# Performance work log

Hardware: AMD Instinct MI355X
Metric: run time of the kernel (lower is better)

Reference implementation:

```python
import jax, jax.numpy as jnp
import numpy as np

B, S, H = 32, 2048, 512

def setup_inputs() -> dict:
    key = jax.random.key(0)
    k1, k2, k3, k4 = jax.random.split(key, 4)
    Y = jax.random.normal(k1, (B, S, H), dtype=jnp.float32)
    mask_Y = jnp.ones((B, S), dtype=jnp.float32)
    W = jax.random.normal(k2, (H, H), dtype=jnp.float32)
    b = jax.random.normal(k3, (H,), dtype=jnp.float32)
    w = jax.random.normal(k4, (H,), dtype=jnp.float32)
    return {"Y": Y, "mask_Y": mask_Y, "W": W, "b": b, "w": w}

def reference(Y, mask_Y, W, b, w):
    # u: [B,S,H] = tanh(Y @ W + b)
    u = jnp.tanh(jnp.einsum('bsh,hd->bsd', Y, W) + b)
    # scores: [B,S] = u . w, masked with large negative additive bias
    scores = jnp.einsum('bsh,h->bs', u, w) - 1000.0 * (1.0 - mask_Y)
    alpha = jax.nn.softmax(scores, axis=1)  # [B,S]
    # c_star: [B,H] = attention-weighted sum of Y
    c_star = jnp.einsum('bs,bsh->bh', alpha, Y)
    return c_star
```

## Files before the change

kernel.cpp:

```cpp
#include <hip/hip_runtime.h>
#include <hip/hip_bf16.h>


#define Bsz 32
#define Ssz 2048
#define Hsz 512
#define Msz (Bsz * Ssz)

using half8   = __attribute__((ext_vector_type(8))) _Float16;
using floatx4 = __attribute__((ext_vector_type(4))) float;

__device__ __forceinline__ void llds16(void* l, const void* g) {
  __builtin_amdgcn_global_load_lds((const __attribute__((address_space(1))) void*)g,
                                   (__attribute__((address_space(3))) void*)l, 16, 0, 0);
}

__device__ __forceinline__ float fast_tanh(float x) {
  const float e = __expf(2.f * x);
  return 1.f - 2.f / (e + 1.f);
}

__global__ __launch_bounds__(256) void wsplit_k(const float* __restrict__ W,
                                                _Float16* __restrict__ Wt) {
  __shared__ float tile[32][33];
  const int bx = blockIdx.x & 15, by = blockIdx.x >> 4;
  const int tx = threadIdx.x & 31, ty = threadIdx.x >> 5;
#pragma unroll
  for (int i = 0; i < 4; ++i)
    tile[ty + 8 * i][tx] = W[(size_t)(by * 32 + ty + 8 * i) * Hsz + bx * 32 + tx];
  __syncthreads();
#pragma unroll
  for (int i = 0; i < 4; ++i) {
    const int n = bx * 32 + ty + 8 * i;
    const int k = by * 32 + tx;
    Wt[(size_t)n * Hsz + k] = (_Float16)tile[tx][ty + 8 * i];
  }
}

__global__ __launch_bounds__(256) void gemm_score_k(const float* __restrict__ Y,
                                                    const _Float16* __restrict__ Wt,
                                                    const float* __restrict__ bvec,
                                                    const float* __restrict__ wvec,
                                                    float* __restrict__ scores4) {
  __shared__ __align__(16) float    As[2 * 128 * 32];
  __shared__ __align__(16) _Float16 Bs[2 * 128 * 32];
  const int tid = threadIdx.x;
  const int lane = tid & 63, wv = tid >> 6;
  const int wr = wv >> 1, wc = wv & 1;
  const int lr = lane & 15, lq = lane >> 4;
  const int g = blockIdx.x;
  const int x = g & 7, q = g >> 3;
  const int nblk = q & 3;
  const int mblk = (q >> 2) * 8 + x;

  floatx4 acc[4][4];
#pragma unroll
  for (int rf = 0; rf < 4; ++rf)
#pragma unroll
    for (int cf = 0; cf < 4; ++cf)
      acc[rf][cf] = (floatx4){0.f, 0.f, 0.f, 0.f};

  const float* aY = Y + (size_t)mblk * 128 * Hsz;
  const _Float16* bW = Wt + (size_t)nblk * 128 * Hsz;

  auto stage = [&](int buf, int it_) {
    const int k0 = it_ * 32;
#pragma unroll
    for (int i = 0; i < 4; ++i) {
      const int cb = i * 256 + wv * 64;
      const int p = cb + lane;
      const int row = p >> 3;
      const int gc = (p & 7) ^ (row & 7);
      llds16(&As[buf * 4096 + cb * 4], aY + (size_t)row * Hsz + k0 + gc * 4);
    }
#pragma unroll
    for (int i = 0; i < 2; ++i) {
      const int cb = i * 256 + wv * 64;
      const int p = cb + lane;
      const int row = p >> 2;
      const int gc = (p & 3) ^ ((row >> 1) & 3);
      llds16(&Bs[buf * 4096 + cb * 8], bW + (size_t)row * Hsz + k0 + gc * 8);
    }
  };

  stage(0, 0);
  __syncthreads();

  for (int it = 0; it < 16; ++it) {
    const int cur = it & 1;
    if (it < 15) stage(cur ^ 1, it + 1);

    const float*    Asb = As + cur * 4096;
    const _Float16* Bsb = Bs + cur * 4096;

    half8 a[4], bf[4];
#pragma unroll
    for (int rf = 0; rf < 4; ++rf) {
      const int ar = wr * 64 + rf * 16 + lr;
      const int s0 = (lq * 2) ^ (ar & 7);
      const float4 flo = *(const float4*)&Asb[ar * 32 + s0 * 4];
      const float4 fhi = *(const float4*)&Asb[ar * 32 + (s0 ^ 1) * 4];
      half8 h;
      h[0] = (_Float16)flo.x; h[1] = (_Float16)flo.y;
      h[2] = (_Float16)flo.z; h[3] = (_Float16)flo.w;
      h[4] = (_Float16)fhi.x; h[5] = (_Float16)fhi.y;
      h[6] = (_Float16)fhi.z; h[7] = (_Float16)fhi.w;
      a[rf] = h;
    }
#pragma unroll
    for (int cf = 0; cf < 4; ++cf) {
      const int nr = wc * 64 + cf * 16 + lr;
      bf[cf] = *(const half8*)&Bsb[nr * 32 + (lq ^ ((nr >> 1) & 3)) * 8];
    }
#pragma unroll
    for (int rf = 0; rf < 4; ++rf)
#pragma unroll
      for (int cf = 0; cf < 4; ++cf)
        acc[rf][cf] = __builtin_amdgcn_mfma_f32_16x16x32_f16(a[rf], bf[cf], acc[rf][cf], 0, 0, 0);

    __syncthreads();
  }

  float bb[4], ww[4];
  const int colbase = nblk * 128 + wc * 64;
#pragma unroll
  for (int cf = 0; cf < 4; ++cf) {
    const int col = colbase + cf * 16 + lr;
    bb[cf] = bvec[col];
    ww[cf] = wvec[col];
  }
  float* red = (float*)As;
#pragma unroll
  for (int rf = 0; rf < 4; ++rf) {
#pragma unroll
    for (int r = 0; r < 4; ++r) {
      float v = 0.f;
#pragma unroll
      for (int cf = 0; cf < 4; ++cf)
        v += fast_tanh(acc[rf][cf][r] + bb[cf]) * ww[cf];
      v += __shfl_xor(v, 1, 16);
      v += __shfl_xor(v, 2, 16);
      v += __shfl_xor(v, 4, 16);
      v += __shfl_xor(v, 8, 16);
      if (lr == 0)
        red[(wr * 64 + rf * 16 + lq * 4 + r) * 2 + wc] = v;
    }
  }
  __syncthreads();
  if (tid < 128)
    scores4[(size_t)nblk * Msz + mblk * 128 + tid] = red[2 * tid] + red[2 * tid + 1];
}

__global__ __launch_bounds__(256) void softmax_k(const float* __restrict__ scores4,
                                                 const float* __restrict__ mask,
                                                 float* __restrict__ alpha) {
  const int b = blockIdx.x, t = threadIdx.x;
  const int lane = t & 63, wv = t >> 6;
  float s[8];
  float mx = -3.4e38f;
#pragma unroll
  for (int i = 0; i < 8; ++i) {
    const int idx = b * Ssz + i * 256 + t;
    float v = scores4[idx] + scores4[Msz + idx] + scores4[2 * Msz + idx] + scores4[3 * Msz + idx];
    v -= 1000.f * (1.f - mask[idx]);
    s[i] = v;
    mx = fmaxf(mx, v);
  }
  for (int off = 32; off > 0; off >>= 1) mx = fmaxf(mx, __shfl_xor(mx, off, 64));
  __shared__ float rm[4], rs[4];
  if (lane == 0) rm[wv] = mx;
  __syncthreads();
  mx = fmaxf(fmaxf(rm[0], rm[1]), fmaxf(rm[2], rm[3]));
  float sum = 0.f;
#pragma unroll
  for (int i = 0; i < 8; ++i) {
    s[i] = __expf(s[i] - mx);
    sum += s[i];
  }
  for (int off = 32; off > 0; off >>= 1) sum += __shfl_xor(sum, off, 64);
  if (lane == 0) rs[wv] = sum;
  __syncthreads();
  sum = rs[0] + rs[1] + rs[2] + rs[3];
  const float inv = 1.f / sum;
#pragma unroll
  for (int i = 0; i < 8; ++i) alpha[b * Ssz + i * 256 + t] = s[i] * inv;
}

__global__ __launch_bounds__(256) void wsum1_k(const float* __restrict__ alpha,
                                               const float* __restrict__ Y,
                                               float* __restrict__ partial) {
  const int b = blockIdx.x >> 5, sc = blockIdx.x & 31;
  const int t = threadIdx.x, lane = t & 63, wv = t >> 6;
  __shared__ float part[4 * 512];
  const int s0 = sc * 64 + wv * 16;
  const float* al = alpha + b * Ssz + s0;
  const float4* Yb = (const float4*)(Y + ((size_t)b * Ssz + s0) * Hsz);
  float a0 = 0.f, a1 = 0.f, a2 = 0.f, a3 = 0.f, a4 = 0.f, a5 = 0.f, a6 = 0.f, a7 = 0.f;
#pragma unroll 4
  for (int r = 0; r < 16; ++r) {
    const float a = al[r];
    const float4 y0 = Yb[r * 128 + lane * 2];
    const float4 y1 = Yb[r * 128 + lane * 2 + 1];
    a0 = fmaf(a, y0.x, a0); a1 = fmaf(a, y0.y, a1);
    a2 = fmaf(a, y0.z, a2); a3 = fmaf(a, y0.w, a3);
    a4 = fmaf(a, y1.x, a4); a5 = fmaf(a, y1.y, a5);
    a6 = fmaf(a, y1.z, a6); a7 = fmaf(a, y1.w, a7);
  }
  part[wv * 512 + 0 * 64 + lane] = a0;
  part[wv * 512 + 1 * 64 + lane] = a1;
  part[wv * 512 + 2 * 64 + lane] = a2;
  part[wv * 512 + 3 * 64 + lane] = a3;
  part[wv * 512 + 4 * 64 + lane] = a4;
  part[wv * 512 + 5 * 64 + lane] = a5;
  part[wv * 512 + 6 * 64 + lane] = a6;
  part[wv * 512 + 7 * 64 + lane] = a7;
  __syncthreads();
#pragma unroll
  for (int i = 0; i < 2; ++i) {
    const int h = i * 256 + t;
    const int idx = (h & 7) * 64 + (h >> 3);
    partial[((size_t)(b * 32 + sc)) * Hsz + h] =
        part[idx] + part[512 + idx] + part[1024 + idx] + part[1536 + idx];
  }
}

__global__ __launch_bounds__(256) void wsum2_k(const float* __restrict__ partial,
                                               float* __restrict__ out) {
  const int b = blockIdx.x >> 1;
  const int h = (blockIdx.x & 1) * 256 + threadIdx.x;
  float s = 0.f;
#pragma unroll 8
  for (int sc = 0; sc < 32; ++sc)
    s += partial[((size_t)(b * 32 + sc)) * Hsz + h];
  out[b * Hsz + h] = s;
}

extern "C" void kernel_launch(void* const* d_in, const int* in_sizes, int n_in,
                              void* d_out, int out_size, void* d_ws, size_t ws_size,
                              hipStream_t stream) {
  (void)in_sizes; (void)n_in; (void)out_size; (void)ws_size;
  const float* Y    = (const float*)d_in[0];
  const float* mask = (const float*)d_in[1];
  const float* W    = (const float*)d_in[2];
  const float* bvec = (const float*)d_in[3];
  const float* wvec = (const float*)d_in[4];
  float* out = (float*)d_out;

  char* ws = (char*)d_ws;
  _Float16* Wt   = (_Float16*)ws;
  float* scores4 = (float*)(ws + ((size_t)1 << 20));
  float* alpha   = (float*)(ws + ((size_t)2 << 20));
  float* partial = (float*)(ws + ((size_t)3 << 20));

  wsplit_k<<<256, 256, 0, stream>>>(W, Wt);
  gemm_score_k<<<(Msz / 128) * 4, 256, 0, stream>>>(Y, Wt, bvec, wvec, scores4);
  softmax_k<<<Bsz, 256, 0, stream>>>(scores4, mask, alpha);
  wsum1_k<<<Bsz * 32, 256, 0, stream>>>(alpha, Y, partial);
  wsum2_k<<<Bsz * 2, 256, 0, stream>>>(partial, out);
}
```

Measured before the change: 288.7 us.

## Prefetch two K-tiles ahead with explicit vmcnt waits and split barriers

Restructures the GEMM main loop's global-to-LDS pipeline so two stages are in flight. Each iteration waits on vmcnt for the older stage, reads fragments to registers, then barriers and issues the next load into the just-freed buffer before the MFMAs. Global addresses are precomputed once and advanced by pointer increments instead of recomputing swizzled offsets each stage. This aims to hide global latency better, at the cost of hand-written waitcnt and barrier logic that must stay correct with the compiler's scheduling.

```diff
diff --git a/kernel.cpp b/kernel.cpp
--- a/kernel.cpp
+++ b/kernel.cpp
@@ -63,35 +63,46 @@
   const float* aY = Y + (size_t)mblk * 128 * Hsz;
   const _Float16* bW = Wt + (size_t)nblk * 128 * Hsz;
 
-  auto stage = [&](int buf, int it_) {
-    const int k0 = it_ * 32;
-#pragma unroll
-    for (int i = 0; i < 4; ++i) {
-      const int cb = i * 256 + wv * 64;
-      const int p = cb + lane;
-      const int row = p >> 3;
-      const int gc = (p & 7) ^ (row & 7);
-      llds16(&As[buf * 4096 + cb * 4], aY + (size_t)row * Hsz + k0 + gc * 4);
-    }
-#pragma unroll
-    for (int i = 0; i < 2; ++i) {
-      const int cb = i * 256 + wv * 64;
-      const int p = cb + lane;
-      const int row = p >> 2;
-      const int gc = (p & 3) ^ ((row >> 1) & 3);
-      llds16(&Bs[buf * 4096 + cb * 8], bW + (size_t)row * Hsz + k0 + gc * 8);
-    }
+  int aLds[4]; const float* aG[4];
+#pragma unroll
+  for (int i = 0; i < 4; ++i) {
+    const int cb = i * 256 + wv * 64;
+    const int p = cb + lane;
+    const int row = p >> 3;
+    const int gc = (p & 7) ^ (row & 7);
+    aLds[i] = cb * 4;
+    aG[i] = aY + (size_t)row * Hsz + gc * 4;
+  }
+  int bLds[2]; const _Float16* bG[2];
+#pragma unroll
+  for (int i = 0; i < 2; ++i) {
+    const int cb = i * 256 + wv * 64;
+    const int p = cb + lane;
+    const int row = p >> 2;
+    const int gc = (p & 3) ^ ((row >> 1) & 3);
+    bLds[i] = cb * 8;
+    bG[i] = bW + (size_t)row * Hsz + gc * 8;
+  }
+
+  auto stage = [&](int bufOff) {
+#pragma unroll
+    for (int i = 0; i < 4; ++i) { llds16(&As[bufOff + aLds[i]], aG[i]); aG[i] += 32; }
+#pragma unroll
+    for (int i = 0; i < 2; ++i) { llds16(&Bs[bufOff + bLds[i]], bG[i]); bG[i] += 32; }
   };
 
-  stage(0, 0);
-  __syncthreads();
+  stage(0);
+  stage(4096);
 
   for (int it = 0; it < 16; ++it) {
-    const int cur = it & 1;
-    if (it < 15) stage(cur ^ 1, it + 1);
-
-    const float*    Asb = As + cur * 4096;
-    const _Float16* Bsb = Bs + cur * 4096;
+    if (it < 15) { asm volatile("s_waitcnt vmcnt(6)" ::: "memory"); }
+    else         { asm volatile("s_waitcnt vmcnt(0)" ::: "memory"); }
+    __builtin_amdgcn_sched_barrier(0);
+    __builtin_amdgcn_s_barrier();
+
+    const int bufOff = (it & 1) * 4096;
+    const float*    Asb = As + bufOff;
+    const _Float16* Bsb = Bs + bufOff;
 
     half8 a[4], bf[4];
 #pragma unroll
@@ -112,13 +123,18 @@
       const int nr = wc * 64 + cf * 16 + lr;
       bf[cf] = *(const half8*)&Bsb[nr * 32 + (lq ^ ((nr >> 1) & 3)) * 8];
     }
+
+    asm volatile("s_waitcnt lgkmcnt(0)" ::: "memory");
+    __builtin_amdgcn_sched_barrier(0);
+    __builtin_amdgcn_s_barrier();
+    __builtin_amdgcn_sched_barrier(0);
+    if (it < 14) stage(bufOff);
+
 #pragma unroll
     for (int rf = 0; rf < 4; ++rf)
 #pragma unroll
       for (int cf = 0; cf < 4; ++cf)
         acc[rf][cf] = __builtin_amdgcn_mfma_f32_16x16x32_f16(a[rf], bf[cf], acc[rf][cf], 0, 0, 0);
-
-    __syncthreads();
   }
 
   float bb[4], ww[4];
```

Result: no change. 284.8 us (-1.3%).
